# Performance work log

Hardware: AMD Instinct MI355X
Metric: run time of the kernel (lower is better)

Reference implementation:

```python
import jax, jax.numpy as jnp
import numpy as np

N_ENC, BATCH = 2048, 32
ENC, DEC, HID = 1024, 1024, 1024
NEG_BIG = 2.0e9


def setup_inputs() -> dict:
    key = jax.random.key(0)
    k1, k2, k3, k4, k5, k6 = jax.random.split(key, 6)
    enc_states = jax.random.normal(k1, (N_ENC, BATCH, ENC), dtype=jnp.float32)
    enc_mask = jax.random.randint(k2, (N_ENC, BATCH), 0, 2).astype(jnp.bool_)
    dec_state = jax.random.normal(k3, (BATCH, DEC), dtype=jnp.float32)
    # nn.Linear weights, stored as [out, in] like torch; kaiming-uniform-ish init
    w_enc = jax.random.uniform(k4, (HID, ENC), dtype=jnp.float32, minval=-1, maxval=1) / np.sqrt(ENC)
    w_dec = jax.random.uniform(k5, (HID, DEC), dtype=jnp.float32, minval=-1, maxval=1) / np.sqrt(DEC)
    w_out = jax.random.uniform(k6, (1, HID), dtype=jnp.float32, minval=-1, maxval=1) / np.sqrt(HID)
    return {"enc_states": enc_states, "enc_mask": enc_mask, "dec_state": dec_state,
            "w_enc": w_enc, "w_dec": w_dec, "w_out": w_out}


def reference(enc_states, enc_mask, dec_state, w_enc, w_dec, w_out):
    # proj_enc: [n_enc, batch, hid];  proj_dec: [batch, hid]
    proj_enc = jnp.einsum('sbe,he->sbh', enc_states, w_enc)
    proj_dec = jnp.einsum('bd,hd->bh', dec_state, w_dec)
    activation = jnp.tanh(proj_enc + proj_dec[None, :, :])
    # logits: [n_enc, batch]
    attn_logits = jnp.einsum('sbh,h->sb', activation, w_out[0])
    m = enc_mask.astype(attn_logits.dtype)
    attn_logits = attn_logits * m - (1.0 - m) * NEG_BIG
    attn_weights = jax.nn.softmax(attn_logits, axis=0)          # softmax over seq dim
    attn_response = jnp.einsum('sbe,sb->be', enc_states, attn_weights)
    return attn_response, attn_weights
```

## Files before the change

### kernel.cpp

```cpp
#include <hip/hip_runtime.h>
#include <hip/hip_bf16.h>
#include <stdint.h>

#define N_ENC 2048
#define BATCH 32
#define M_TOT (N_ENC * BATCH)
#define K_DIM 1024
#define N_DIM 1024
#define BK 64
#define NT (K_DIM / BK)
#define NSLAB 16

typedef __attribute__((ext_vector_type(4))) float f32x4;
typedef __attribute__((ext_vector_type(8))) short short8;

__device__ __forceinline__ unsigned int pack_bf16x2(float lo, float hi) {
  unsigned int a = __float_as_uint(lo);
  unsigned int b = __float_as_uint(hi);
  a = (a + 0x7fffu + ((a >> 16) & 1u)) >> 16;
  b = (b + 0x7fffu + ((b >> 16) & 1u)) & 0xffff0000u;
  return a | b;
}

__device__ __forceinline__ float bf2f(unsigned short u) {
  return __uint_as_float((unsigned int)u << 16);
}

__device__ __forceinline__ float tanh_fast(float x) {
  float e = __expf(2.0f * x);
  return 1.0f - 2.0f / (e + 1.0f);
}

__device__ __forceinline__ int mask_mode_detect(const void* maskp, int t,
                                                int* mf) {
  if (t < 2) mf[t] = 0;
  __syncthreads();
  unsigned w0 = ((const unsigned*)maskp)[t & 255];
  if (t < 256) {
    if (w0 == 0x3f800000u) mf[1] = 1;
    else if (w0 > 1u) mf[0] = 1;
  }
  __syncthreads();
  return mf[1] ? 2 : (mf[0] ? 1 : 0);
}

__device__ __forceinline__ int mask_read(const void* maskp, int mode, int idx) {
  if (mode == 0) return ((const int*)maskp)[idx] != 0;
  if (mode == 1) return ((const unsigned char*)maskp)[idx] != 0;
  return ((const float*)maskp)[idx] != 0.f;
}

__global__ __launch_bounds__(256) void k_count(const void* __restrict__ maskp,
                                               int* __restrict__ bcnt) {
  const int t = threadIdx.x, lane = t & 63, wv = t >> 6;
  __shared__ int mf[2];
  __shared__ int ws_[4];
  const int mode = mask_mode_detect(maskp, t, mf);
  const int idx = blockIdx.x * 256 + t;
  int mk = mask_read(maskp, mode, idx);
  unsigned long long bal = __ballot(mk);
  if (lane == 0) ws_[wv] = __popcll(bal);
  __syncthreads();
  if (t == 0) bcnt[blockIdx.x] = ws_[0] + ws_[1] + ws_[2] + ws_[3];
}

__global__ __launch_bounds__(256) void k_fill(const void* __restrict__ maskp,
                                              const int* __restrict__ bcnt,
                                              int* __restrict__ pos,
                                              int* __restrict__ ridx,
                                              int* __restrict__ mcount) {
  const int t = threadIdx.x, lane = t & 63, wv = t >> 6;
  __shared__ int mf[2];
  __shared__ int sc[256];
  __shared__ int wtot[4];
  __shared__ int wcnt[4];
  const int mode = mask_mode_detect(maskp, t, mf);

  int x = bcnt[t];
#pragma unroll
  for (int d = 1; d < 64; d <<= 1) {
    int y = __shfl_up(x, d);
    if (lane >= d) x += y;
  }
  if (lane == 63) wtot[wv] = x;
  __syncthreads();
  int add = 0;
  for (int i = 0; i < wv; ++i) add += wtot[i];
  sc[t] = x + add;
  __syncthreads();
  const int blockoff = blockIdx.x ? sc[blockIdx.x - 1] : 0;
  if (blockIdx.x == 0 && t == 0) *mcount = sc[255];

  const int idx = blockIdx.x * 256 + t;
  int mk = mask_read(maskp, mode, idx);
  unsigned long long bal = __ballot(mk);
  int lpfx = __popcll(bal & ((1ULL << lane) - 1ULL));
  if (lane == 0) wcnt[wv] = __popcll(bal);
  __syncthreads();
  int wb = 0;
  for (int i = 0; i < wv; ++i) wb += wcnt[i];
  int off = blockoff + wb + lpfx;
  if (mk) { pos[idx] = off; ridx[off] = idx; }
  else pos[idx] = -1;
}

__global__ void k_gather_cvt(const float* __restrict__ enc,
                             const int* __restrict__ ridx,
                             const int* __restrict__ mcount,
                             unsigned short* __restrict__ cmp) {
  const int mc = *mcount;
  const int e = threadIdx.x * 4;
  for (int j = blockIdx.x; j < mc; j += gridDim.x) {
    const int row = ridx[j];
    f32x4 v = *(const f32x4*)(enc + (size_t)row * K_DIM + e);
    uint2 o;
    o.x = pack_bf16x2(v.x, v.y);
    o.y = pack_bf16x2(v.z, v.w);
    *(uint2*)(cmp + (size_t)j * K_DIM + e) = o;
  }
}

__global__ void k_convert_bf16(const float* __restrict__ src,
                               unsigned short* __restrict__ dst, int n8) {
  for (int i = blockIdx.x * 256 + threadIdx.x; i < n8; i += gridDim.x * 256) {
    const float* p = src + (size_t)i * 8;
    f32x4 v0 = *(const f32x4*)p;
    f32x4 v1 = *(const f32x4*)(p + 4);
    uint4 o;
    o.x = pack_bf16x2(v0.x, v0.y);
    o.y = pack_bf16x2(v0.z, v0.w);
    o.z = pack_bf16x2(v1.x, v1.y);
    o.w = pack_bf16x2(v1.z, v1.w);
    *(uint4*)(dst + (size_t)i * 8) = o;
  }
}

__global__ void k_proj_dec(const float* __restrict__ dec,
                           const float* __restrict__ w_dec,
                           float* __restrict__ proj) {
  int t = threadIdx.x;
  int hh = t & 7, b = t >> 3;
  int h = blockIdx.x * 8 + hh;
  const float* wr = w_dec + (size_t)h * K_DIM;
  const float* dr = dec + (size_t)b * K_DIM;
  float acc = 0.f;
  for (int d = 0; d < K_DIM; d += 4) {
    f32x4 wv = *(const f32x4*)(wr + d);
    f32x4 dv = *(const f32x4*)(dr + d);
    acc = fmaf(wv.x, dv.x, acc);
    acc = fmaf(wv.y, dv.y, acc);
    acc = fmaf(wv.z, dv.z, acc);
    acc = fmaf(wv.w, dv.w, acc);
  }
  proj[b * N_DIM + h] = acc;
}

__global__ __launch_bounds__(256, 3) void k_gemm128(
    const unsigned short* __restrict__ Abf,
    const unsigned short* __restrict__ B,
    const int* __restrict__ ridx,
    const int* __restrict__ mcount,
    const float* __restrict__ pdec,
    const float* __restrict__ wout,
    float* __restrict__ lp)
{
  __shared__ __align__(16) unsigned short Asm[128 * BK];
  __shared__ __align__(16) unsigned short Bsm[128 * BK];

  const int mc = *mcount;
  const int mtiles = (mc + 127) >> 7;
  const int T = mtiles * 8;
  if ((int)blockIdx.x >= T) return;
  const int swz = ((int)blockIdx.x % 8) * mtiles + (int)blockIdx.x / 8;
  const int nt8 = swz & 7;
  const int mt = swz >> 3;
  const int m0 = mt * 128, n0 = nt8 * 128;

  const int t = threadIdx.x;
  const int lane = t & 63;
  const int w = t >> 6;
  const int wm = w >> 1, wn = w & 1;
  const int g = lane >> 4, c16 = lane & 15;

  f32x4 acc[4][4];
#pragma unroll
  for (int a = 0; a < 4; ++a)
#pragma unroll
    for (int b = 0; b < 4; ++b) acc[a][b] = {0.f, 0.f, 0.f, 0.f};

  const unsigned short* gA[4];
  const unsigned short* gB[4];
#pragma unroll
  for (int r = 0; r < 4; ++r) {
    int item = r * 256 + t;
    int row = item >> 3;
    int sub = (item & 7) ^ (row & 7);
    gA[r] = Abf + (size_t)(m0 + row) * K_DIM + sub * 8;
    gB[r] = B   + (size_t)(n0 + row) * K_DIM + sub * 8;
  }

  for (int kt = 0; kt < NT; ++kt) {
#pragma unroll
    for (int r = 0; r < 4; ++r) {
      __builtin_amdgcn_global_load_lds(
          (const __attribute__((address_space(1))) void*)gA[r],
          (__attribute__((address_space(3))) void*)&Asm[(r * 256 + t) * 8],
          16, 0, 0);
      gA[r] += BK;
      __builtin_amdgcn_global_load_lds(
          (const __attribute__((address_space(1))) void*)gB[r],
          (__attribute__((address_space(3))) void*)&Bsm[(r * 256 + t) * 8],
          16, 0, 0);
      gB[r] += BK;
    }
    __syncthreads();
#pragma unroll
    for (int ks = 0; ks < 2; ++ks) {
      const int sub = ks * 4 + g;
      short8 af[4], bfr[4];
#pragma unroll
      for (int a = 0; a < 4; ++a) {
        int row = wm * 64 + a * 16 + c16;
        af[a] = *(const short8*)&Asm[row * 64 + ((sub ^ (row & 7)) * 8)];
      }
#pragma unroll
      for (int b = 0; b < 4; ++b) {
        int row = wn * 64 + b * 16 + c16;
        bfr[b] = *(const short8*)&Bsm[row * 64 + ((sub ^ (row & 7)) * 8)];
      }
#pragma unroll
      for (int a = 0; a < 4; ++a)
#pragma unroll
        for (int b = 0; b < 4; ++b)
          acc[a][b] = __builtin_amdgcn_mfma_f32_16x16x32_bf16(
              af[a], bfr[b], acc[a][b], 0, 0, 0);
    }
    __syncthreads();
  }

  float* slab = lp + (size_t)(nt8 * 2 + wn) * M_TOT;
#pragma unroll
  for (int a = 0; a < 4; ++a) {
    int brow[4];
#pragma unroll
    for (int j = 0; j < 4; ++j) {
      int cj = m0 + wm * 64 + a * 16 + g * 4 + j;
      brow[j] = (cj < mc) ? (ridx[cj] & 31) : 0;
    }
    float psum[4] = {0.f, 0.f, 0.f, 0.f};
#pragma unroll
    for (int b = 0; b < 4; ++b) {
      const int col = n0 + wn * 64 + b * 16 + c16;
      const float wo = wout[col];
#pragma unroll
      for (int j = 0; j < 4; ++j) {
        float v = acc[a][b][j] + pdec[brow[j] * N_DIM + col];
        psum[j] = fmaf(tanh_fast(v), wo, psum[j]);
      }
    }
#pragma unroll
    for (int j = 0; j < 4; ++j) {
      float p = psum[j];
      p += __shfl_xor(p, 1);
      p += __shfl_xor(p, 2);
      p += __shfl_xor(p, 4);
      p += __shfl_xor(p, 8);
      if (c16 == 0)
        slab[m0 + wm * 64 + a * 16 + g * 4 + j] = p;
    }
  }
}

__global__ void k_sumslab(const float* __restrict__ lp,
                          const int* __restrict__ mcount,
                          float* __restrict__ lsum) {
  const int mc = *mcount;
  for (int i = blockIdx.x * 256 + threadIdx.x; i < mc; i += gridDim.x * 256) {
    float s = 0.f;
#pragma unroll
    for (int k = 0; k < NSLAB; ++k) s += lp[(size_t)k * M_TOT + i];
    lsum[i] = s;
  }
}

__global__ __launch_bounds__(256) void k_gemm_f32(
    const float* __restrict__ A,
    const unsigned short* __restrict__ B,
    const float* __restrict__ pdec,
    const float* __restrict__ wout,
    float* __restrict__ lp)
{
  __shared__ __align__(16) unsigned short Asm[128 * BK];
  __shared__ __align__(16) unsigned short Bsm[128 * BK];
  const int bid = blockIdx.x;
  const int nt8 = bid & 7;
  const int mt = bid >> 3;
  const int m0 = mt * 128, n0 = nt8 * 128;
  const int t = threadIdx.x;
  const int lane = t & 63;
  const int w = t >> 6;
  const int wm = w >> 1, wn = w & 1;
  const int g = lane >> 4, c16 = lane & 15;

  f32x4 acc[4][4];
#pragma unroll
  for (int a = 0; a < 4; ++a)
#pragma unroll
    for (int b = 0; b < 4; ++b) acc[a][b] = {0.f, 0.f, 0.f, 0.f};

  for (int kt = 0; kt < NT; ++kt) {
    const int k0 = kt * BK;
#pragma unroll
    for (int i = 0; i < 4; ++i) {
      int item = i * 256 + t;
      int row = item >> 3;
      int sub = item & 7;
      const float* src = A + (size_t)(m0 + row) * K_DIM + k0 + sub * 8;
      f32x4 v0 = *(const f32x4*)src;
      f32x4 v1 = *(const f32x4*)(src + 4);
      uint4 o;
      o.x = pack_bf16x2(v0.x, v0.y);
      o.y = pack_bf16x2(v0.z, v0.w);
      o.z = pack_bf16x2(v1.x, v1.y);
      o.w = pack_bf16x2(v1.z, v1.w);
      int chunk = sub ^ (row & 7);
      *(uint4*)&Asm[row * 64 + chunk * 8] = o;
    }
#pragma unroll
    for (int j = 0; j < 4; ++j) {
      int chunkid = w * 4 + j;
      int item = chunkid * 64 + lane;
      int row = item >> 3;
      int sub = (item & 7) ^ (row & 7);
      const unsigned short* gp = B + (size_t)(n0 + row) * K_DIM + k0 + sub * 8;
      __builtin_amdgcn_global_load_lds(
          (const __attribute__((address_space(1))) void*)gp,
          (__attribute__((address_space(3))) void*)&Bsm[chunkid * 512],
          16, 0, 0);
    }
    __syncthreads();
#pragma unroll
    for (int ks = 0; ks < 2; ++ks) {
      const int sub = ks * 4 + g;
      short8 af[4], bfr[4];
#pragma unroll
      for (int a = 0; a < 4; ++a) {
        int row = wm * 64 + a * 16 + c16;
        af[a] = *(const short8*)&Asm[row * 64 + ((sub ^ (row & 7)) * 8)];
      }
#pragma unroll
      for (int b = 0; b < 4; ++b) {
        int row = wn * 64 + b * 16 + c16;
        bfr[b] = *(const short8*)&Bsm[row * 64 + ((sub ^ (row & 7)) * 8)];
      }
#pragma unroll
      for (int a = 0; a < 4; ++a)
#pragma unroll
        for (int b = 0; b < 4; ++b)
          acc[a][b] = __builtin_amdgcn_mfma_f32_16x16x32_bf16(
              af[a], bfr[b], acc[a][b], 0, 0, 0);
    }
    __syncthreads();
  }
  float* slab = lp + (size_t)(nt8 * 2 + wn) * M_TOT;
#pragma unroll
  for (int a = 0; a < 4; ++a) {
    float psum[4] = {0.f, 0.f, 0.f, 0.f};
#pragma unroll
    for (int b = 0; b < 4; ++b) {
      const int col = n0 + wn * 64 + b * 16 + c16;
      const float wo = wout[col];
#pragma unroll
      for (int j = 0; j < 4; ++j) {
        const int rl = wm * 64 + a * 16 + g * 4 + j;
        const int bidx = rl & 31;
        float v = acc[a][b][j] + pdec[bidx * N_DIM + col];
        psum[j] = fmaf(tanh_fast(v), wo, psum[j]);
      }
    }
#pragma unroll
    for (int j = 0; j < 4; ++j) {
      float p = psum[j];
      p += __shfl_xor(p, 1);
      p += __shfl_xor(p, 2);
      p += __shfl_xor(p, 4);
      p += __shfl_xor(p, 8);
      if (c16 == 0)
        slab[m0 + wm * 64 + a * 16 + g * 4 + j] = p;
    }
  }
}

template <bool GATHER>
__global__ void k_softmax(const float* __restrict__ lsrc,
                          const int* __restrict__ pos,
                          const void* __restrict__ maskp,
                          float* __restrict__ weights) {
  const int b = blockIdx.x;
  const int t = threadIdx.x;
  const int lane = t & 63, wid = t >> 6;
  __shared__ float red[8];
  __shared__ int mf[2];

  int mode = 0;
  if (!GATHER) mode = mask_mode_detect(maskp, t, mf);

  float v[8];
  float mx = -3.0e38f;
#pragma unroll
  for (int i = 0; i < 8; ++i) {
    int idx = (t + i * 256) * BATCH + b;
    float l;
    if (GATHER) {
      int p = pos[idx];
      l = (p >= 0) ? lsrc[p] : -2.0e9f;
    } else {
      l = 0.f;
#pragma unroll
      for (int k = 0; k < NSLAB; ++k) l += lsrc[(size_t)k * M_TOT + idx];
      l = mask_read(maskp, mode, idx) ? l : -2.0e9f;
    }
    v[i] = l;
    mx = fmaxf(mx, l);
  }
#pragma unroll
  for (int off = 1; off < 64; off <<= 1) mx = fmaxf(mx, __shfl_xor(mx, off));
  if (lane == 0) red[wid] = mx;
  __syncthreads();
  mx = fmaxf(fmaxf(red[0], red[1]), fmaxf(red[2], red[3]));

  float sum = 0.f;
#pragma unroll
  for (int i = 0; i < 8; ++i) {
    float e = __expf(v[i] - mx);
    v[i] = e;
    sum += e;
  }
#pragma unroll
  for (int off = 1; off < 64; off <<= 1) sum += __shfl_xor(sum, off);
  if (lane == 0) red[4 + wid] = sum;
  __syncthreads();
  sum = red[4] + red[5] + red[6] + red[7];
  float inv = 1.0f / sum;
#pragma unroll
  for (int i = 0; i < 8; ++i)
    weights[(t + i * 256) * BATCH + b] = v[i] * inv;
}

__global__ void k_response2(const float* __restrict__ enc,
                            const unsigned short* __restrict__ cmp,
                            const int* __restrict__ pos,
                            const float* __restrict__ weights,
                            float* __restrict__ out) {
  const int b = blockIdx.x & 31;
  const int ch = blockIdx.x >> 5;
  const int e = threadIdx.x * 4;
  float a0 = 0.f, a1 = 0.f, a2 = 0.f, a3 = 0.f;
  const int s0 = ch * (N_ENC / 16);
  for (int s = s0; s < s0 + N_ENC / 16; ++s) {
    const int idx = s * BATCH + b;
    float wv = weights[idx];
    if (wv != 0.f) {
      int p = pos[idx];
      if (p >= 0) {
        ushort4 x = *(const ushort4*)(cmp + (size_t)p * K_DIM + e);
        a0 = fmaf(wv, bf2f(x.x), a0);
        a1 = fmaf(wv, bf2f(x.y), a1);
        a2 = fmaf(wv, bf2f(x.z), a2);
        a3 = fmaf(wv, bf2f(x.w), a3);
      } else {
        f32x4 x = *(const f32x4*)(enc + (size_t)idx * K_DIM + e);
        a0 = fmaf(wv, x.x, a0);
        a1 = fmaf(wv, x.y, a1);
        a2 = fmaf(wv, x.z, a2);
        a3 = fmaf(wv, x.w, a3);
      }
    }
  }
  atomicAdd(&out[b * K_DIM + e + 0], a0);
  atomicAdd(&out[b * K_DIM + e + 1], a1);
  atomicAdd(&out[b * K_DIM + e + 2], a2);
  atomicAdd(&out[b * K_DIM + e + 3], a3);
}

__global__ void k_response(const float* __restrict__ enc,
                           const float* __restrict__ weights,
                           float* __restrict__ out) {
  const int b = blockIdx.x & 31;
  const int ch = blockIdx.x >> 5;
  const int e = threadIdx.x * 4;
  float a0 = 0.f, a1 = 0.f, a2 = 0.f, a3 = 0.f;
  const int s0 = ch * (N_ENC / 16);
  for (int s = s0; s < s0 + N_ENC / 16; ++s) {
    float wv = weights[s * BATCH + b];
    f32x4 x = *(const f32x4*)(enc + ((size_t)s * BATCH + b) * K_DIM + e);
    a0 = fmaf(wv, x.x, a0);
    a1 = fmaf(wv, x.y, a1);
    a2 = fmaf(wv, x.z, a2);
    a3 = fmaf(wv, x.w, a3);
  }
  atomicAdd(&out[b * K_DIM + e + 0], a0);
  atomicAdd(&out[b * K_DIM + e + 1], a1);
  atomicAdd(&out[b * K_DIM + e + 2], a2);
  atomicAdd(&out[b * K_DIM + e + 3], a3);
}

extern "C" void kernel_launch(void* const* d_in, const int* in_sizes, int n_in,
                              void* d_out, int out_size, void* d_ws, size_t ws_size,
                              hipStream_t stream) {
  const float* enc   = (const float*)d_in[0];
  const void*  mask  = d_in[1];
  const float* dec   = (const float*)d_in[2];
  const float* w_enc = (const float*)d_in[3];
  const float* w_dec = (const float*)d_in[4];
  const float* w_out = (const float*)d_in[5];

  float* out_resp = (float*)d_out;
  float* out_w    = out_resp + BATCH * K_DIM;

  const size_t cmp_bytes = (size_t)M_TOT * K_DIM * 2;
  const size_t tail = 2 * 1024 * 1024 + 128 * 1024 +
                      (size_t)NSLAB * M_TOT * 4 +
                      (size_t)M_TOT * 4 * 3 + 8192;
  const bool pre = ws_size >= cmp_bytes + tail;

  char* wsB = (char*)d_ws;
  unsigned short* cmp = (unsigned short*)wsB;
  size_t off = pre ? cmp_bytes : 0;
  unsigned short* w_enc_bf = (unsigned short*)(wsB + off);     off += 2 * 1024 * 1024;
  float* pdec = (float*)(wsB + off);                           off += 128 * 1024;
  float* lp   = (float*)(wsB + off);                           off += (size_t)NSLAB * M_TOT * 4;
  int* pos    = (int*)(wsB + off);                             off += (size_t)M_TOT * 4;
  int* ridx   = (int*)(wsB + off);                             off += (size_t)M_TOT * 4;
  float* lsum = (float*)(wsB + off);                           off += (size_t)M_TOT * 4;
  int* bcnt   = (int*)(wsB + off);                             off += 1024 * 4;
  int* mcount = (int*)(wsB + off);

  hipMemsetAsync(out_resp, 0, (size_t)BATCH * K_DIM * sizeof(float), stream);

  k_convert_bf16<<<512, 256, 0, stream>>>(w_enc, w_enc_bf, N_DIM * K_DIM / 8);
  k_proj_dec<<<N_DIM / 8, 256, 0, stream>>>(dec, w_dec, pdec);

  if (pre) {
    k_count<<<M_TOT / 256, 256, 0, stream>>>(mask, bcnt);
    k_fill<<<M_TOT / 256, 256, 0, stream>>>(mask, bcnt, pos, ridx, mcount);
    k_gather_cvt<<<2048, 256, 0, stream>>>(enc, ridx, mcount, cmp);
    k_gemm128<<<(M_TOT / 128) * (N_DIM / 128), 256, 0, stream>>>(
        cmp, w_enc_bf, ridx, mcount, pdec, w_out, lp);
    k_sumslab<<<256, 256, 0, stream>>>(lp, mcount, lsum);
    k_softmax<true><<<BATCH, 256, 0, stream>>>(lsum, pos, mask, out_w);
    k_response2<<<BATCH * 16, 256, 0, stream>>>(enc, cmp, pos, out_w, out_resp);
  } else {
    k_gemm_f32<<<(M_TOT / 128) * (N_DIM / 128), 256, 0, stream>>>(
        enc, w_enc_bf, pdec, w_out, lp);
    k_softmax<false><<<BATCH, 256, 0, stream>>>(lp, pos, mask, out_w);
    k_response<<<BATCH * 16, 256, 0, stream>>>(enc, out_w, out_resp);
  }
}
```

Before: 248.1 us.

## Split response reduction by column chunks with in-block sequence halves, drop atomics

The response kernel now gives each block 128 output columns for one batch entry and splits the sequence into two halves handled by the two halves of the block. The halves are combined through shared memory and written directly, so the atomics and the memset of the output are no longer needed on this path. Each thread now loads a single scalar element per step instead of a 4-wide vector, and the grid shrinks from 512 to 256 blocks, which may lower memory-level parallelism on the weighted gather.

```diff
diff --git a/kernel.cpp b/kernel.cpp
--- a/kernel.cpp
+++ b/kernel.cpp
@@ -447,40 +447,35 @@
     weights[(t + i * 256) * BATCH + b] = v[i] * inv;
 }
 
-__global__ void k_response2(const float* __restrict__ enc,
-                            const unsigned short* __restrict__ cmp,
-                            const int* __restrict__ pos,
-                            const float* __restrict__ weights,
-                            float* __restrict__ out) {
+__global__ __launch_bounds__(256) void k_response3(
+    const float* __restrict__ enc,
+    const unsigned short* __restrict__ cmp,
+    const int* __restrict__ pos,
+    const float* __restrict__ weights,
+    float* __restrict__ out) {
   const int b = blockIdx.x & 31;
-  const int ch = blockIdx.x >> 5;
-  const int e = threadIdx.x * 4;
-  float a0 = 0.f, a1 = 0.f, a2 = 0.f, a3 = 0.f;
-  const int s0 = ch * (N_ENC / 16);
-  for (int s = s0; s < s0 + N_ENC / 16; ++s) {
+  const int q = blockIdx.x >> 5;
+  const int t = threadIdx.x;
+  const int cl = t & 127;
+  const int sh = t >> 7;
+  const int col = q * 128 + cl;
+  __shared__ float partial[256];
+
+  float acc = 0.f;
+  const int s0 = sh * (N_ENC / 2);
+  for (int s = s0; s < s0 + N_ENC / 2; ++s) {
     const int idx = s * BATCH + b;
-    float wv = weights[idx];
+    const float wv = weights[idx];
     if (wv != 0.f) {
-      int p = pos[idx];
-      if (p >= 0) {
-        ushort4 x = *(const ushort4*)(cmp + (size_t)p * K_DIM + e);
-        a0 = fmaf(wv, bf2f(x.x), a0);
-        a1 = fmaf(wv, bf2f(x.y), a1);
-        a2 = fmaf(wv, bf2f(x.z), a2);
-        a3 = fmaf(wv, bf2f(x.w), a3);
-      } else {
-        f32x4 x = *(const f32x4*)(enc + (size_t)idx * K_DIM + e);
-        a0 = fmaf(wv, x.x, a0);
-        a1 = fmaf(wv, x.y, a1);
-        a2 = fmaf(wv, x.z, a2);
-        a3 = fmaf(wv, x.w, a3);
-      }
-    }
-  }
-  atomicAdd(&out[b * K_DIM + e + 0], a0);
-  atomicAdd(&out[b * K_DIM + e + 1], a1);
-  atomicAdd(&out[b * K_DIM + e + 2], a2);
-  atomicAdd(&out[b * K_DIM + e + 3], a3);
+      const int p = pos[idx];
+      float x = (p >= 0) ? bf2f(cmp[(size_t)p * K_DIM + col])
+                         : enc[(size_t)idx * K_DIM + col];
+      acc = fmaf(wv, x, acc);
+    }
+  }
+  partial[t] = acc;
+  __syncthreads();
+  if (t < 128) out[b * K_DIM + col] = partial[t] + partial[t + 128];
 }
 
 __global__ void k_response(const float* __restrict__ enc,
@@ -536,8 +531,6 @@
   int* bcnt   = (int*)(wsB + off);                             off += 1024 * 4;
   int* mcount = (int*)(wsB + off);
 
-  hipMemsetAsync(out_resp, 0, (size_t)BATCH * K_DIM * sizeof(float), stream);
-
   k_convert_bf16<<<512, 256, 0, stream>>>(w_enc, w_enc_bf, N_DIM * K_DIM / 8);
   k_proj_dec<<<N_DIM / 8, 256, 0, stream>>>(dec, w_dec, pdec);
 
@@ -549,8 +542,9 @@
         cmp, w_enc_bf, ridx, mcount, pdec, w_out, lp);
     k_sumslab<<<256, 256, 0, stream>>>(lp, mcount, lsum);
     k_softmax<true><<<BATCH, 256, 0, stream>>>(lsum, pos, mask, out_w);
-    k_response2<<<BATCH * 16, 256, 0, stream>>>(enc, cmp, pos, out_w, out_resp);
+    k_response3<<<BATCH * 8, 256, 0, stream>>>(enc, cmp, pos, out_w, out_resp);
   } else {
+    hipMemsetAsync(out_resp, 0, (size_t)BATCH * K_DIM * sizeof(float), stream);
     k_gemm_f32<<<(M_TOT / 128) * (N_DIM / 128), 256, 0, stream>>>(
         enc, w_enc_bf, pdec, w_out, lp);
     k_softmax<false><<<BATCH, 256, 0, stream>>>(lp, pos, mask, out_w);
```

New measurement: 583.5 us. +135.2%, slower.
